# Kernel tuning notes

Hardware: AMD Instinct MI355X
Metric: run time of the kernel (lower is better)

The kernel has to match this reference:

```python
import jax, jax.numpy as jnp
import numpy as np
from jax import lax

STRIDE = 4

def grid_sample_nearest(feat, grid):
    # feat: (B, C, H, W); grid: (B, Ho, Wo, 2) normalized to [-1, 1], align_corners=True,
    # mode='nearest', padding_mode='zeros' (matches torch.nn.functional.grid_sample).
    B, C, H, W = feat.shape
    gx = (grid[..., 0] + 1.0) * 0.5 * (W - 1)
    gy = (grid[..., 1] + 1.0) * 0.5 * (H - 1)
    ix = jnp.round(gx).astype(jnp.int32)  # round-half-to-even == std::nearbyint
    iy = jnp.round(gy).astype(jnp.int32)
    valid = (ix >= 0) & (ix < W) & (iy >= 0) & (iy < H)
    ixc = jnp.clip(ix, 0, W - 1)
    iyc = jnp.clip(iy, 0, H - 1)
    out = jax.vmap(lambda f, y, x: f[:, y, x])(feat, iyc, ixc)  # (B, C, Ho, Wo)
    return out * valid[:, None, :, :].astype(feat.dtype)

def unfold_s(x, s):
    # F.unfold(x, kernel=(s,s), stride=s): (n,c,h,w) -> (n, c*s*s, h//s * w//s)
    n, c, h, w = x.shape
    h4, w4 = h // s, w // s
    x = x.reshape(n, c, h4, s, w4, s).transpose(0, 1, 3, 5, 2, 4)  # (n,c,kh,kw,h4,w4)
    return x.reshape(n, c * s * s, h4 * w4)

def fold_s(x, s, c, h, w):
    # F.fold, kernel=(s,s), stride=s (non-overlapping): (n, c*s*s, h4*w4) -> (n,c,h,w)
    n = x.shape[0]
    h4, w4 = h // s, w // s
    x = x.reshape(n, c, s, s, h4, w4).transpose(0, 1, 4, 2, 5, 3)  # (n,c,h4,kh,w4,kw)
    return x.reshape(n, c, h, w)

def _normalize(x, axis):
    return x / jnp.maximum(jnp.linalg.norm(x, axis=axis, keepdims=True), 1e-12)

def ltam_forward(curr_feat, index_feat_set_s1, anchor_feat, sparse_feat_set_s1,
                 sparse_feat_set_s2, sparse_feat_set_s3, location_feat,
                 fusion_w, fusion_b):
    s = STRIDE
    n, c, h, w = anchor_feat.shape
    t = sparse_feat_set_s1.shape[1]
    h4, w4 = h // s, w // s
    feat_len = c * s * s
    feat_num = h4 * w4

    # build normalized nearest-sampling grid from location map
    gf = location_feat.reshape(n, t, 2, h4, w4).transpose(0, 1, 3, 4, 2)  # (n,t,h4,w4,2)
    gx = 2.0 * gf[..., 0] / max(w4 - 1, 1) - 1.0
    gy = 2.0 * gf[..., 1] / max(h4 - 1, 1) - 1.0
    grid = jnp.stack([gx, gy], axis=-1).reshape(n * t, h4, w4, 2)

    def warp(fs):
        return grid_sample_nearest(fs.reshape(n * t, feat_len, h4, w4), grid)

    out_s1 = warp(sparse_feat_set_s1)   # (n*t, feat_len, h4, w4)
    out_s2 = warp(sparse_feat_set_s2)
    out_s3 = warp(sparse_feat_set_s3)
    idx_s1 = warp(index_feat_set_s1)

    # current-frame patch tokens, L2-normalized
    cf = unfold_s(curr_feat, s).transpose(0, 2, 1)          # (n, feat_num, feat_len)
    cf = _normalize(cf, axis=2)

    # index tokens per frame, L2-normalized, correlate with current tokens
    idx_tok = idx_s1.reshape(n, t, feat_len, feat_num).transpose(0, 3, 1, 2)  # (n,feat_num,t,feat_len)
    idx_tok = _normalize(idx_tok, axis=3)
    matrix_index = jnp.einsum('nptf,npf->npt', idx_tok, cf)  # (n, feat_num, t)

    corr_soft = jnp.max(matrix_index, axis=2)                # (n, feat_num)
    corr_index = jnp.argmax(matrix_index, axis=2)            # (n, feat_num)

    corr_soft_map = fold_s(jnp.broadcast_to(corr_soft[:, None, :], (n, feat_len, feat_num)),
                           s, c, h, w)                       # (n, c, h, w)

    def gather_fold(o):
        o = o.reshape(n, t, feat_len, feat_num)
        idx = jnp.broadcast_to(corr_index[:, None, None, :], (n, 1, feat_len, feat_num))
        g = jnp.take_along_axis(o, idx, axis=1)[:, 0]        # (n, feat_len, feat_num)
        return fold_s(g, s, c, h, w)

    f1 = gather_fold(out_s1)
    f2 = gather_fold(out_s2)
    f3 = gather_fold(out_s3)

    out = jnp.concatenate([f1, f2, f3], axis=1)              # (n, 3c, h, w)
    out = lax.conv_general_dilated(out, fusion_w, (1, 1), ((1, 1), (1, 1)),
                                   dimension_numbers=('NCHW', 'OIHW', 'NCHW'))
    out = out + fusion_b[None, :, None, None]
    out = out * corr_soft_map + anchor_feat
    return out

def setup_inputs() -> dict:
    key = jax.random.key(0)
    ks = jax.random.split(key, 10)
    n, t, c, h, w, s = 1, 4, 128, 192, 192, STRIDE
    h4, w4 = h // s, w // s
    feat_len = c * s * s
    inp = {
        'curr_feat': jax.random.normal(ks[0], (n, c, h, w), jnp.float32),
        'index_feat_set_s1': jax.random.normal(ks[1], (n, t, feat_len, h4, w4), jnp.float32),
        'anchor_feat': jax.random.normal(ks[2], (n, c, h, w), jnp.float32),
        'sparse_feat_set_s1': jax.random.normal(ks[3], (n, t, feat_len, h4, w4), jnp.float32),
        'sparse_feat_set_s2': jax.random.normal(ks[4], (n, t, feat_len, h4, w4), jnp.float32),
        'sparse_feat_set_s3': jax.random.normal(ks[5], (n, t, feat_len, h4, w4), jnp.float32),
        # unnormalized pixel coordinates in [0, dim-1] (h4 == w4 here)
        'location_feat': jax.random.uniform(ks[6], (n, 2 * t, h4, w4), jnp.float32) * (w4 - 1),
        'fusion_w': jax.random.normal(ks[7], (c, 3 * c, 3, 3), jnp.float32) * 0.02,
        'fusion_b': jax.random.normal(ks[8], (c,), jnp.float32) * 0.02,
    }
    return inp

def reference(curr_feat, index_feat_set_s1, anchor_feat, sparse_feat_set_s1,
              sparse_feat_set_s2, sparse_feat_set_s3, location_feat,
              fusion_w, fusion_b):
    return ltam_forward(curr_feat, index_feat_set_s1, anchor_feat, sparse_feat_set_s1,
                        sparse_feat_set_s2, sparse_feat_set_s3, location_feat,
                        fusion_w, fusion_b)
```

## Files before the change

### kernel.cpp

```cpp
#include <hip/hip_runtime.h>
#include <hip/hip_bf16.h>
#include <math.h>

#define T_FRAMES 4
#define C 128
#define H 192
#define W 192
#define H4 48
#define W4 48
#define FEAT_LEN 2048
#define FEAT_NUM 2304
#define HW (H*W)
#define NCH 384
#define KTOT 3456
#define NSTEP 54
#define PPX 194

typedef __bf16 bf16x8 __attribute__((ext_vector_type(8)));
typedef float f32x4 __attribute__((ext_vector_type(4)));

__device__ __forceinline__ void gl16(const void* gp, void* ldsbase) {
    __builtin_amdgcn_global_load_lds(
        (const __attribute__((address_space(1))) void*)gp,
        (__attribute__((address_space(3))) void*)ldsbase, 16, 0, 0);
}

__device__ __forceinline__ void sample_loc(const float* __restrict__ loc, int k, int p,
                                           int& iy, int& ix, int& valid) {
    float gfx = loc[(2*k+0)*FEAT_NUM + p];
    float gfy = loc[(2*k+1)*FEAT_NUM + p];
    float gx = 2.0f*gfx/47.0f - 1.0f;
    float gy = 2.0f*gfy/47.0f - 1.0f;
    float fx = (gx + 1.0f)*0.5f*47.0f;
    float fy = (gy + 1.0f)*0.5f*47.0f;
    int jx = (int)rintf(fx);
    int jy = (int)rintf(fy);
    valid = (jx >= 0 && jx < W4 && jy >= 0 && jy < H4) ? 1 : 0;
    ix = min(max(jx, 0), W4-1);
    iy = min(max(jy, 0), H4-1);
}

__global__ __launch_bounds__(256) void k_tr(const float* __restrict__ src,
                                            float* __restrict__ dst) {
    __shared__ float lds[64*65];
    int p0 = blockIdx.x*64, f0 = blockIdx.y*64, k = blockIdx.z;
    const float* s = src + (size_t)k*FEAT_LEN*FEAT_NUM;
    float* d = dst + (size_t)k*FEAT_NUM*FEAT_LEN;
    int tid = threadIdx.x;
    int pl = tid & 63, fb = tid >> 6;
#pragma unroll
    for (int i = 0; i < 16; ++i) {
        int fl = fb*16 + i;
        lds[fl*65 + pl] = s[(size_t)(f0+fl)*FEAT_NUM + p0 + pl];
    }
    __syncthreads();
    int f4 = (tid & 15)*4, pb = tid >> 4;
#pragma unroll
    for (int i = 0; i < 4; ++i) {
        int pl2 = pb + i*16;
        float4 v = { lds[(f4+0)*65 + pl2], lds[(f4+1)*65 + pl2],
                     lds[(f4+2)*65 + pl2], lds[(f4+3)*65 + pl2] };
        *(float4*)&d[(size_t)(p0+pl2)*FEAT_LEN + f0 + f4] = v;
    }
}

__global__ __launch_bounds__(256) void k_trs(const float* __restrict__ s1,
                                             const float* __restrict__ s2,
                                             const float* __restrict__ s3,
                                             ushort* __restrict__ spT) {
    __shared__ float lds[64*65];
    int p0 = blockIdx.x*64, f0 = blockIdx.y*64;
    int z = blockIdx.z;
    int set = z >> 2, k = z & 3;
    const float* src = (set == 0) ? s1 : ((set == 1) ? s2 : s3);
    const float* s = src + (size_t)k*FEAT_LEN*FEAT_NUM;
    int tid = threadIdx.x;
    int pl = tid & 63, fb = tid >> 6;
#pragma unroll
    for (int i = 0; i < 16; ++i) {
        int fl = fb*16 + i;
        lds[fl*65 + pl] = s[(size_t)(f0+fl)*FEAT_NUM + p0 + pl];
    }
    __syncthreads();
    int fo = (tid & 7)*8, pr = tid >> 3;
#pragma unroll
    for (int i = 0; i < 2; ++i) {
        int row = pr + i*32;
        ushort vv[8];
#pragma unroll
        for (int j = 0; j < 8; ++j) {
            __hip_bfloat16 b = __float2bfloat16(lds[(fo+j)*65 + row]);
            vv[j] = *(ushort*)&b;
        }
        uint4 pk;
        pk.x = (uint)vv[0] | ((uint)vv[1] << 16);
        pk.y = (uint)vv[2] | ((uint)vv[3] << 16);
        pk.z = (uint)vv[4] | ((uint)vv[5] << 16);
        pk.w = (uint)vv[6] | ((uint)vv[7] << 16);
        *(uint4*)(spT + ((size_t)z*FEAT_NUM + p0 + row)*FEAT_LEN + f0 + fo) = pk;
    }
}

__global__ __launch_bounds__(256) void k_gather2(const ushort* __restrict__ spT,
                                                 const float* __restrict__ loc,
                                                 const int* __restrict__ corr_index,
                                                 ushort* __restrict__ cat) {
    __shared__ ushort tok[3*FEAT_LEN];
    int p = blockIdx.x;
    int y4 = p / W4, x4 = p - y4*W4;
    int tid = threadIdx.x;
    int k = corr_index[p];
    int iy, ix, valid;
    sample_loc(loc, k, p, iy, ix, valid);
    int sp = iy*W4 + ix;

#pragma unroll
    for (int j = 0; j < 3; ++j) {
        int idx = j*256 + tid;
        int set = idx >> 8, off = (idx & 255)*8;
        uint4 v = {0u,0u,0u,0u};
        if (valid)
            v = *(const uint4*)(spT + ((size_t)(set*4 + k)*FEAT_NUM + sp)*FEAT_LEN + off);
        *(uint4*)(tok + set*FEAT_LEN + off) = v;
    }
    __syncthreads();

#pragma unroll
    for (int j = 0; j < 3; ++j) {
        int idx = j*256 + tid;
        int px16 = idx / 48, oct = idx - px16*48;
        int ky = px16 >> 2, kx = px16 & 3;
        int y = y4*4 + ky, x = x4*4 + kx;
        int set = oct >> 4, c0 = (oct & 15)*8;
        int sub = (ky << 2) + kx;
        ushort vv[8];
#pragma unroll
        for (int e = 0; e < 8; ++e) vv[e] = tok[set*FEAT_LEN + ((c0 + e) << 4) + sub];
        uint4 pk;
        pk.x = (uint)vv[0] | ((uint)vv[1] << 16);
        pk.y = (uint)vv[2] | ((uint)vv[3] << 16);
        pk.z = (uint)vv[4] | ((uint)vv[5] << 16);
        pk.w = (uint)vv[6] | ((uint)vv[7] << 16);
        *(uint4*)(cat + ((size_t)(y+1)*PPX + (x+1))*NCH + set*128 + c0) = pk;
    }
}

__global__ __launch_bounds__(256) void k_corr2(const float* __restrict__ curr,
                                               const float* __restrict__ idxT,
                                               const float* __restrict__ loc,
                                               int* __restrict__ corr_index,
                                               float* __restrict__ corr_soft) {
    int p = blockIdx.x;
    int y4 = p / W4, x4 = p - y4*W4;
    int tid = threadIdx.x;

    int iy[T_FRAMES], ix[T_FRAMES], valid[T_FRAMES];
    const float* tok[T_FRAMES];
#pragma unroll
    for (int k = 0; k < T_FRAMES; ++k) {
        sample_loc(loc, k, p, iy[k], ix[k], valid[k]);
        tok[k] = idxT + ((size_t)k*FEAT_NUM + iy[k]*W4 + ix[k])*FEAT_LEN;
    }

    float ss_cf = 0.f;
    float dotk[T_FRAMES] = {0.f,0.f,0.f,0.f};
    float ssk[T_FRAMES]  = {0.f,0.f,0.f,0.f};
    int ybase = y4*4, xbase = x4*4;

#pragma unroll
    for (int it = 0; it < 2; ++it) {
        int f4 = (tid + it*256)*4;
        int cc = f4 >> 4, kh = (f4 >> 2) & 3;
        float4 cf = *(const float4*)&curr[cc*HW + (ybase+kh)*W + xbase];
        ss_cf += cf.x*cf.x + cf.y*cf.y + cf.z*cf.z + cf.w*cf.w;
#pragma unroll
        for (int k = 0; k < T_FRAMES; ++k) {
            if (valid[k]) {
                float4 v = *(const float4*)&tok[k][f4];
                dotk[k] += cf.x*v.x + cf.y*v.y + cf.z*v.z + cf.w*v.w;
                ssk[k]  += v.x*v.x + v.y*v.y + v.z*v.z + v.w*v.w;
            }
        }
    }

    float vals[9] = {ss_cf, dotk[0],dotk[1],dotk[2],dotk[3], ssk[0],ssk[1],ssk[2],ssk[3]};
#pragma unroll
    for (int j = 0; j < 9; ++j) {
        float v = vals[j];
#pragma unroll
        for (int off = 32; off > 0; off >>= 1) v += __shfl_xor(v, off, 64);
        vals[j] = v;
    }
    __shared__ float red[4][9];
    int wave = tid >> 6, lane = tid & 63;
    if (lane == 0) {
#pragma unroll
        for (int j = 0; j < 9; ++j) red[wave][j] = vals[j];
    }
    __syncthreads();
    if (tid == 0) {
        float tot[9];
#pragma unroll
        for (int j = 0; j < 9; ++j) tot[j] = red[0][j]+red[1][j]+red[2][j]+red[3][j];
        float ncf = fmaxf(sqrtf(tot[0]), 1e-12f);
        float best = -1e30f; int bestk = 0;
#pragma unroll
        for (int k = 0; k < T_FRAMES; ++k) {
            float nk = fmaxf(sqrtf(tot[5+k]), 1e-12f);
            float m = tot[1+k] / (nk * ncf);
            if (m > best) { best = m; bestk = k; }
        }
        corr_index[p] = bestk;
        corr_soft[p]  = best;
    }
}

__global__ __launch_bounds__(256) void k_corr(const float* __restrict__ curr,
                                              const float* __restrict__ idxf,
                                              const float* __restrict__ loc,
                                              int* __restrict__ corr_index,
                                              float* __restrict__ corr_soft) {
    int p = blockIdx.x;
    int y4 = p / W4, x4 = p - y4*W4;
    int tid = threadIdx.x;

    int iy[T_FRAMES], ix[T_FRAMES], valid[T_FRAMES];
#pragma unroll
    for (int k = 0; k < T_FRAMES; ++k) sample_loc(loc, k, p, iy[k], ix[k], valid[k]);

    float ss_cf = 0.f;
    float dotk[T_FRAMES] = {0.f,0.f,0.f,0.f};
    float ssk[T_FRAMES]  = {0.f,0.f,0.f,0.f};

    int ybase = y4*4, xbase = x4*4;
    for (int f = tid; f < FEAT_LEN; f += 256) {
        int cc = f >> 4;
        int kh = (f >> 2) & 3;
        int kw = f & 3;
        float cf = curr[cc*HW + (ybase+kh)*W + (xbase+kw)];
        ss_cf += cf*cf;
#pragma unroll
        for (int k = 0; k < T_FRAMES; ++k) {
            float v = 0.f;
            if (valid[k]) v = idxf[(k*FEAT_LEN + f)*FEAT_NUM + iy[k]*W4 + ix[k]];
            dotk[k] += cf*v;
            ssk[k]  += v*v;
        }
    }

    float vals[9] = {ss_cf, dotk[0],dotk[1],dotk[2],dotk[3], ssk[0],ssk[1],ssk[2],ssk[3]};
#pragma unroll
    for (int j = 0; j < 9; ++j) {
        float v = vals[j];
#pragma unroll
        for (int off = 32; off > 0; off >>= 1) v += __shfl_xor(v, off, 64);
        vals[j] = v;
    }
    __shared__ float red[4][9];
    int wave = tid >> 6, lane = tid & 63;
    if (lane == 0) {
#pragma unroll
        for (int j = 0; j < 9; ++j) red[wave][j] = vals[j];
    }
    __syncthreads();
    if (tid == 0) {
        float tot[9];
#pragma unroll
        for (int j = 0; j < 9; ++j) tot[j] = red[0][j]+red[1][j]+red[2][j]+red[3][j];
        float ncf = fmaxf(sqrtf(tot[0]), 1e-12f);
        float best = -1e30f; int bestk = 0;
#pragma unroll
        for (int k = 0; k < T_FRAMES; ++k) {
            float nk = fmaxf(sqrtf(tot[5+k]), 1e-12f);
            float m = tot[1+k] / (nk * ncf);
            if (m > best) { best = m; bestk = k; }
        }
        corr_index[p] = bestk;
        corr_soft[p]  = best;
    }
}

__global__ __launch_bounds__(256) void k_wconv(const float* __restrict__ w,
                                               ushort* __restrict__ wt) {
    int gid = blockIdx.x*256 + threadIdx.x;
    if (gid >= 128*KTOT) return;
    int o = gid / KTOT, rem = gid - o*KTOT;
    int step = rem >> 6, ci = rem & 63;
    int chunk = step / 9, tap = step - chunk*9;
    int ci_g = chunk*64 + ci;
    __hip_bfloat16 b = __float2bfloat16(w[(o*NCH + ci_g)*9 + tap]);
    wt[gid] = *(ushort*)&b;
}

__global__ __launch_bounds__(256) void k_border(ushort* __restrict__ cat) {
    int gid = blockIdx.x*256 + threadIdx.x;
    if (gid >= 772*48) return;
    int oct = gid % 48, bp = gid / 48;
    int ypad, xpad;
    if (bp < 194)      { ypad = 0;        xpad = bp; }
    else if (bp < 388) { ypad = 193;      xpad = bp - 194; }
    else if (bp < 580) { ypad = bp - 387; xpad = 0; }
    else               { ypad = bp - 579; xpad = 193; }
    uint4 z = {0u,0u,0u,0u};
    *(uint4*)(cat + (ypad*PPX + xpad)*NCH + oct*8) = z;
}

__global__ __launch_bounds__(256) void k_gather(const float* __restrict__ s1,
                                                const float* __restrict__ s2,
                                                const float* __restrict__ s3,
                                                const float* __restrict__ loc,
                                                const int* __restrict__ corr_index,
                                                ushort* __restrict__ cat) {
    int gid = blockIdx.x*256 + threadIdx.x;
    if (gid >= HW*48) return;
    int oct = gid % 48, px = gid / 48;
    int x = px % W, y = px / W;
    int p = (y >> 2)*W4 + (x >> 2);
    int k = corr_index[p];
    int iy, ix, valid;
    sample_loc(loc, k, p, iy, ix, valid);
    int set = oct >> 4;
    int c0  = (oct & 15) * 8;
    int sub = ((y & 3) << 2) + (x & 3);
    ushort v[8];
#pragma unroll
    for (int e = 0; e < 8; ++e) v[e] = 0;
    if (valid) {
        const float* src = (set == 0) ? s1 : ((set == 1) ? s2 : s3);
        const float* sp = src + (size_t)k*FEAT_LEN*FEAT_NUM + iy*W4 + ix;
#pragma unroll
        for (int e = 0; e < 8; ++e) {
            int f = ((c0 + e) << 4) + sub;
            __hip_bfloat16 b = __float2bfloat16(sp[(size_t)f*FEAT_NUM]);
            v[e] = *(ushort*)&b;
        }
    }
    uint4 pk;
    pk.x = (uint)v[0] | ((uint)v[1] << 16);
    pk.y = (uint)v[2] | ((uint)v[3] << 16);
    pk.z = (uint)v[4] | ((uint)v[5] << 16);
    pk.w = (uint)v[6] | ((uint)v[7] << 16);
    *(uint4*)(cat + ((y+1)*PPX + (x+1))*NCH + oct*8) = pk;
}

__global__ __launch_bounds__(256, 2) void k_conv2(const ushort* __restrict__ cat,
                                                  const ushort* __restrict__ wt,
                                                  const float* __restrict__ bias,
                                                  const float* __restrict__ corr_soft,
                                                  const float* __restrict__ anchor,
                                                  float* __restrict__ out) {
    __shared__ char smX[2][136*128];
    __shared__ char smW[2][128*128];

    int tx = blockIdx.x, ty = blockIdx.y;
    int tid = threadIdx.x;
    int wave = tid >> 6, l = tid & 63;
    int lx = l & 15, lg = l >> 4;
    int co0w = wave * 32;
    int kpart = lg * 16;
    int wbofs = (wave*64)*16;

    auto stageW = [&](int step, int b) {
#pragma unroll
        for (int q = 0; q < 4; ++q) {
            int idx = tid + q*256;
            int col = idx >> 3, oct = idx & 7;
            int octp = oct ^ (col & 7);
            const ushort* gp = wt + ((size_t)col*NSTEP + step)*64 + octp*8;
            gl16(gp, smW[b] + q*256*16 + wbofs);
        }
    };
    auto stageX = [&](int chunk, int b) {
#pragma unroll
        for (int q = 0; q < 4; ++q) {
            int idx = tid + q*256;
            int rc = idx >> 3, oct = idx & 7;
            int r = rc / 34, xp = rc - r*34;
            int octp = oct ^ (xp & 7);
            const ushort* gp = cat + ((size_t)(ty*2 + r)*PPX + (tx*32 + xp))*NCH
                               + chunk*64 + octp*8;
            gl16(gp, smX[b] + q*256*16 + wbofs);
        }
        if (wave == 0) {
            int idx = 1024 + l;
            int rc = idx >> 3, oct = idx & 7;
            int xp = rc - 102;
            int octp = oct ^ (xp & 7);
            const ushort* gp = cat + ((size_t)(ty*2 + 3)*PPX + (tx*32 + xp))*NCH
                               + chunk*64 + octp*8;
            gl16(gp, smX[0] + 1024*16 + (b ? (int)sizeof(smX[0]) : 0));
        }
    };

    f32x4 acc[2][4];
#pragma unroll
    for (int mf = 0; mf < 2; ++mf)
#pragma unroll
        for (int nf = 0; nf < 4; ++nf) acc[mf][nf] = (f32x4){0.f,0.f,0.f,0.f};

    int pyv[4], pxxv[4];
#pragma unroll
    for (int nf = 0; nf < 4; ++nf) { int pxl = nf*16 + lx; pyv[nf] = pxl >> 5; pxxv[nf] = pxl & 31; }
    int wbase[2], wswz[2];
#pragma unroll
    for (int mf = 0; mf < 2; ++mf) { int col = co0w + mf*16 + lx; wbase[mf] = col*128; wswz[mf] = (col & 7) << 4; }

    stageX(0, 0);
    stageW(0, 0);
    __syncthreads();

    for (int chunk = 0; chunk < 6; ++chunk) {
        const char* Xb = smX[chunk & 1];
#pragma unroll
        for (int tap = 0; tap < 9; ++tap) {
            int step = chunk*9 + tap;
            const char* Wb = smW[step & 1];
            if (step < NSTEP-1) stageW(step+1, (step+1) & 1);
            if (tap == 8 && chunk < 5) stageX(chunk+1, (chunk+1) & 1);

            const int dy = tap/3 - 1, dx = tap%3 - 1;
            int xrc[4], xsw[4];
#pragma unroll
            for (int nf = 0; nf < 4; ++nf) {
                int xp2 = pxxv[nf] + dx + 1;
                xrc[nf] = (pyv[nf] + dy + 1)*34 + xp2;
                xsw[nf] = (xp2 & 7) << 4;
            }
#pragma unroll
            for (int kk = 0; kk < 2; ++kk) {
                int kb = kk*64 + kpart;
                bf16x8 wf[2], xf[4];
#pragma unroll
                for (int mf = 0; mf < 2; ++mf)
                    wf[mf] = *(const bf16x8*)(Wb + wbase[mf] + (kb ^ wswz[mf]));
#pragma unroll
                for (int nf = 0; nf < 4; ++nf)
                    xf[nf] = *(const bf16x8*)(Xb + xrc[nf]*128 + (kb ^ xsw[nf]));
#pragma unroll
                for (int mf = 0; mf < 2; ++mf)
#pragma unroll
                    for (int nf = 0; nf < 4; ++nf)
                        acc[mf][nf] = __builtin_amdgcn_mfma_f32_16x16x32_bf16(
                            wf[mf], xf[nf], acc[mf][nf], 0, 0, 0);
            }
            __syncthreads();
        }
    }

    float cs[4]; int pixo[4];
#pragma unroll
    for (int nf = 0; nf < 4; ++nf) {
        int y = ty*2 + pyv[nf];
        int x = tx*32 + pxxv[nf];
        cs[nf] = corr_soft[(ty >> 1)*W4 + (x >> 2)];
        pixo[nf] = y*W + x;
    }
#pragma unroll
    for (int mf = 0; mf < 2; ++mf) {
#pragma unroll
        for (int j = 0; j < 4; ++j) {
            int co = co0w + mf*16 + lg*4 + j;
            float b = bias[co];
#pragma unroll
            for (int nf = 0; nf < 4; ++nf) {
                int o = co*HW + pixo[nf];
                out[o] = (acc[mf][nf][j] + b)*cs[nf] + anchor[o];
            }
        }
    }
}

extern "C" void kernel_launch(void* const* d_in, const int* in_sizes, int n_in,
                              void* d_out, int out_size, void* d_ws, size_t ws_size,
                              hipStream_t stream) {
    const float* curr   = (const float*)d_in[0];
    const float* idxf   = (const float*)d_in[1];
    const float* anchor = (const float*)d_in[2];
    const float* s1     = (const float*)d_in[3];
    const float* s2     = (const float*)d_in[4];
    const float* s3     = (const float*)d_in[5];
    const float* loc    = (const float*)d_in[6];
    const float* wgt    = (const float*)d_in[7];
    const float* bias   = (const float*)d_in[8];
    float* out = (float*)d_out;

    char* ws = (char*)d_ws;
    int*    corr_index = (int*)ws;
    float*  corr_soft  = (float*)(ws + 16384);
    ushort* wt         = (ushort*)(ws + 32768);
    ushort* cat        = (ushort*)(ws + 917504);
    char*   big        = ws + 917504 + 28912128;
    float*  idxT       = (float*)big;
    ushort* spT        = (ushort*)big;
    const size_t SPT_BYTES  = (size_t)3*T_FRAMES*FEAT_NUM*FEAT_LEN*2;
    const size_t IDXT_BYTES = (size_t)T_FRAMES*FEAT_NUM*FEAT_LEN*4;
    const size_t NEED_A = 29829632 + (SPT_BYTES > IDXT_BYTES ? SPT_BYTES : IDXT_BYTES);
    const size_t NEED_B = 917504 + IDXT_BYTES;

    if (ws_size >= NEED_A) {
        hipLaunchKernelGGL(k_tr, dim3(36, 32, 4), dim3(256), 0, stream, idxf, idxT);
        hipLaunchKernelGGL(k_corr2, dim3(FEAT_NUM), dim3(256), 0, stream,
                           curr, idxT, loc, corr_index, corr_soft);
        hipLaunchKernelGGL(k_wconv, dim3((128*KTOT + 255)/256), dim3(256), 0, stream, wgt, wt);
        hipLaunchKernelGGL(k_border, dim3((772*48 + 255)/256), dim3(256), 0, stream, cat);
        hipLaunchKernelGGL(k_trs, dim3(36, 32, 12), dim3(256), 0, stream, s1, s2, s3, spT);
        hipLaunchKernelGGL(k_gather2, dim3(FEAT_NUM), dim3(256), 0, stream,
                           spT, loc, corr_index, cat);
    } else {
        float*  idxT_b = (float*)(ws + 917504);
        ushort* cat_b  = (ushort*)(ws + 917504);
        if (ws_size >= NEED_B) {
            hipLaunchKernelGGL(k_tr, dim3(36, 32, 4), dim3(256), 0, stream, idxf, idxT_b);
            hipLaunchKernelGGL(k_corr2, dim3(FEAT_NUM), dim3(256), 0, stream,
                               curr, idxT_b, loc, corr_index, corr_soft);
        } else {
            hipLaunchKernelGGL(k_corr, dim3(FEAT_NUM), dim3(256), 0, stream,
                               curr, idxf, loc, corr_index, corr_soft);
        }
        hipLaunchKernelGGL(k_wconv, dim3((128*KTOT + 255)/256), dim3(256), 0, stream, wgt, wt);
        hipLaunchKernelGGL(k_border, dim3((772*48 + 255)/256), dim3(256), 0, stream, cat_b);
        hipLaunchKernelGGL(k_gather, dim3((HW*48 + 255)/256), dim3(256), 0, stream,
                           s1, s2, s3, loc, corr_index, cat_b);
        hipLaunchKernelGGL(k_conv2, dim3(6, 96), dim3(256), 0, stream,
                           cat_b, wt, bias, corr_soft, anchor, out);
        return;
    }
    hipLaunchKernelGGL(k_conv2, dim3(6, 96), dim3(256), 0, stream,
                       cat, wt, bias, corr_soft, anchor, out);
}
```

Before: 245.6 us.

## Load conv weights directly into registers and sync once per chunk

In the fusion conv kernel, weight fragments are now read straight from global memory (expected to hit in cache) into registers for each tap, instead of being staged through a double-buffered LDS tile. This removes the weight LDS buffer and its per-tap staging, and lets the block barrier move from every tap to once per input-channel chunk. The next X chunk is now prefetched at the start of each chunk rather than at the last tap. In exchange, each tap waits on global or cache latency for its weights without explicit prefetching, which could stall the MFMA pipeline.

```diff
diff --git a/kernel.cpp b/kernel.cpp
--- a/kernel.cpp
+++ b/kernel.cpp
@@ -350,27 +350,16 @@
                                                   const float* __restrict__ anchor,
                                                   float* __restrict__ out) {
     __shared__ char smX[2][136*128];
-    __shared__ char smW[2][128*128];
 
     int tx = blockIdx.x, ty = blockIdx.y;
     int tid = threadIdx.x;
     int wave = tid >> 6, l = tid & 63;
     int lx = l & 15, lg = l >> 4;
     int co0w = wave * 32;
-    int kpart = lg * 16;
     int wbofs = (wave*64)*16;
 
-    auto stageW = [&](int step, int b) {
-#pragma unroll
-        for (int q = 0; q < 4; ++q) {
-            int idx = tid + q*256;
-            int col = idx >> 3, oct = idx & 7;
-            int octp = oct ^ (col & 7);
-            const ushort* gp = wt + ((size_t)col*NSTEP + step)*64 + octp*8;
-            gl16(gp, smW[b] + q*256*16 + wbofs);
-        }
-    };
     auto stageX = [&](int chunk, int b) {
+        char* xb = (char*)smX[b];
 #pragma unroll
         for (int q = 0; q < 4; ++q) {
             int idx = tid + q*256;
@@ -379,7 +368,7 @@
             int octp = oct ^ (xp & 7);
             const ushort* gp = cat + ((size_t)(ty*2 + r)*PPX + (tx*32 + xp))*NCH
                                + chunk*64 + octp*8;
-            gl16(gp, smX[b] + q*256*16 + wbofs);
+            gl16(gp, xb + q*256*16 + wbofs);
         }
         if (wave == 0) {
             int idx = 1024 + l;
@@ -388,7 +377,7 @@
             int octp = oct ^ (xp & 7);
             const ushort* gp = cat + ((size_t)(ty*2 + 3)*PPX + (tx*32 + xp))*NCH
                                + chunk*64 + octp*8;
-            gl16(gp, smX[0] + 1024*16 + (b ? (int)sizeof(smX[0]) : 0));
+            gl16(gp, xb + 1024*16);
         }
     };
 
@@ -401,24 +390,29 @@
     int pyv[4], pxxv[4];
 #pragma unroll
     for (int nf = 0; nf < 4; ++nf) { int pxl = nf*16 + lx; pyv[nf] = pxl >> 5; pxxv[nf] = pxl & 31; }
-    int wbase[2], wswz[2];
-#pragma unroll
-    for (int mf = 0; mf < 2; ++mf) { int col = co0w + mf*16 + lx; wbase[mf] = col*128; wswz[mf] = (col & 7) << 4; }
+    const ushort* wcol[2];
+#pragma unroll
+    for (int mf = 0; mf < 2; ++mf) {
+        int col = co0w + mf*16 + lx;
+        wcol[mf] = wt + (size_t)col*KTOT + lg*8;
+    }
 
     stageX(0, 0);
-    stageW(0, 0);
     __syncthreads();
 
     for (int chunk = 0; chunk < 6; ++chunk) {
+        if (chunk < 5) stageX(chunk+1, (chunk+1) & 1);
         const char* Xb = smX[chunk & 1];
 #pragma unroll
         for (int tap = 0; tap < 9; ++tap) {
-            int step = chunk*9 + tap;
-            const char* Wb = smW[step & 1];
-            if (step < NSTEP-1) stageW(step+1, (step+1) & 1);
-            if (tap == 8 && chunk < 5) stageX(chunk+1, (chunk+1) & 1);
-
+            const int step = chunk*9 + tap;
             const int dy = tap/3 - 1, dx = tap%3 - 1;
+            bf16x8 wf[2][2];
+#pragma unroll
+            for (int mf = 0; mf < 2; ++mf)
+#pragma unroll
+                for (int kk = 0; kk < 2; ++kk)
+                    wf[mf][kk] = *(const bf16x8*)(wcol[mf] + step*64 + kk*32);
             int xrc[4], xsw[4];
 #pragma unroll
             for (int nf = 0; nf < 4; ++nf) {
@@ -428,11 +422,8 @@
             }
 #pragma unroll
             for (int kk = 0; kk < 2; ++kk) {
-                int kb = kk*64 + kpart;
-                bf16x8 wf[2], xf[4];
-#pragma unroll
-                for (int mf = 0; mf < 2; ++mf)
-                    wf[mf] = *(const bf16x8*)(Wb + wbase[mf] + (kb ^ wswz[mf]));
+                int kb = kk*64 + lg*16;
+                bf16x8 xf[4];
 #pragma unroll
                 for (int nf = 0; nf < 4; ++nf)
                     xf[nf] = *(const bf16x8*)(Xb + xrc[nf]*128 + (kb ^ xsw[nf]));
@@ -441,10 +432,10 @@
 #pragma unroll
                     for (int nf = 0; nf < 4; ++nf)
                         acc[mf][nf] = __builtin_amdgcn_mfma_f32_16x16x32_bf16(
-                            wf[mf], xf[nf], acc[mf][nf], 0, 0, 0);
+                            wf[mf][kk], xf[nf], acc[mf][nf], 0, 0, 0);
             }
-            __syncthreads();
-        }
+        }
+        __syncthreads();
     }
 
     float cs[4]; int pixo[4];
```

New measurement: 240.5 us. -2.1%, faster.
